# Optimization experiments

Measured on AMD Instinct MI355X. Metric: run time of the kernel, lower is better.

## Reference

```python
import jax, jax.numpy as jnp
import numpy as np

N_HID = 4
EPS = 1e-6  # LayerNorm eps (note: added to std, torch-style, std with ddof=1)


def _rnn_layer(wx_out, prev_pre, uh, g, b):
    """Sequential recurrence: at = wx_out[k] + h @ Uh^T; skip-subtract prev pre-act;
    custom layernorm (gamma*(x-mean)/(std+eps)+beta, std unbiased); relu.
    Returns (hiddens [T,B,H], pre_acts [T,B,H])."""
    T, B, H = wx_out.shape

    def step(h, inp):
        wx_k, prev_k = inp
        at = wx_k + h @ uh.T          # [B,H]
        pre = at
        a = at - prev_k               # skip connection (subtract prev layer pre-act)
        mean = a.mean(-1, keepdims=True)
        std = jnp.std(a, axis=-1, ddof=1, keepdims=True)
        a = g * (a - mean) / (std + EPS) + b
        h_new = jax.nn.relu(a)        # drop_mask = 1-drop_rate = 1.0 (test mode, drop_rate=0)
        return h_new, (h_new, pre)

    h0 = jnp.zeros((B, H), wx_out.dtype)
    _, (hs, pres) = jax.lax.scan(step, h0, (wx_out, prev_pre))
    return hs, pres


def setup_inputs() -> dict:
    key = jax.random.key(0)
    ks = jax.random.split(key, 12)
    T, B, D, H, C = 400, 32, 440, 1024, 3500
    s = 0.02
    return {
        "x": jax.random.normal(ks[0], (T, B, D), dtype=jnp.float32),
        "lab": jax.random.randint(ks[1], (T, B), 0, C),
        "test_flag": 1,
        "wx0_w": jax.random.normal(ks[2], (H, D), dtype=jnp.float32) * s,
        "wx0_b": jnp.zeros((H,), jnp.float32),
        "wx_w": jax.random.normal(ks[3], (N_HID - 1, H, H), dtype=jnp.float32) * s,
        "wx_b": jnp.zeros((N_HID - 1, H), jnp.float32),
        "uh_w": jax.random.normal(ks[4], (N_HID, H, H), dtype=jnp.float32) * s,
        "ln_g": jnp.ones((N_HID, H), jnp.float32),
        "ln_b": jnp.zeros((N_HID, H), jnp.float32),
        "fco_w": jax.random.normal(ks[5], (C, H), dtype=jnp.float32) * s,
        "fco_b": jnp.zeros((C,), jnp.float32),
    }


def reference(x, lab, test_flag, wx0_w, wx0_b, wx_w, wx_b, uh_w, ln_g, ln_b, fco_w, fco_b):
    T, B, _ = x.shape
    H = uh_w.shape[-1]
    prev_pre = jnp.zeros((T, B, H), x.dtype)  # skip_conn: layer 0 subtracts zeros
    h = x
    for i in range(N_HID):
        if i == 0:
            wx_out = jnp.einsum('tbd,hd->tbh', h, wx0_w) + wx0_b
        else:
            wx_out = jnp.einsum('tbd,hd->tbh', h, wx_w[i - 1]) + wx_b[i - 1]
        h, prev_pre = _rnn_layer(wx_out, prev_pre, uh_w[i], ln_g[i], ln_b[i])
    out = jnp.einsum('tbh,ch->tbc', h, fco_w) + fco_b   # [T,B,C]
    pout = jax.nn.log_softmax(out, axis=2)
    pred = jnp.argmax(pout, axis=2)
    nll = -jnp.take_along_axis(pout, lab[..., None], axis=2).squeeze(-1)
    loss = nll.mean()
    err = jnp.mean((pred != lab).astype(jnp.float32))
    return loss, err, pout
```

## Files before the change

kernel.cpp:

```cpp
#include <hip/hip_runtime.h>
#include <math.h>

#define T_STEPS 400
#define BATCH   32
#define HID     1024
#define MROWS   (T_STEPS * BATCH)
#define NCLS    3500
#define NG      8
#define BPG     4
#define CPG     32
#define JS      32
#define EPS     1e-6f
#define SLOTP   8

typedef __attribute__((ext_vector_type(8))) short short8v;
typedef __attribute__((ext_vector_type(4))) float f32x4;

__device__ __forceinline__ unsigned short bf16_rne(float x) {
  unsigned u = __builtin_bit_cast(unsigned, x);
  unsigned r = u + 0x7FFFu + ((u >> 16) & 1u);
  return (unsigned short)(r >> 16);
}

__device__ __forceinline__ void stage_tile(
    const float* __restrict__ src, int rowlim, int row0, int ld,
    int k0, int K, unsigned short* hi, unsigned short* lo, int tid) {
  #pragma unroll
  for (int it = 0; it < 2; ++it) {
    const int task = tid + 256 * it;
    const int r = task >> 2, q = task & 3;
    const int gr = row0 + r;
    const bool rok = gr < rowlim;
    const float* p = src + (size_t)gr * ld + k0 + q * 8;
    float x[8];
    if (rok && (k0 + 32 <= K)) {
      float4 v0 = *(const float4*)p;
      float4 v1 = *(const float4*)(p + 4);
      x[0] = v0.x; x[1] = v0.y; x[2] = v0.z; x[3] = v0.w;
      x[4] = v1.x; x[5] = v1.y; x[6] = v1.z; x[7] = v1.w;
    } else {
      #pragma unroll
      for (int j = 0; j < 8; ++j)
        x[j] = (rok && (k0 + q * 8 + j) < K) ? p[j] : 0.f;
    }
    unsigned hp[4], lp[4];
    #pragma unroll
    for (int j = 0; j < 4; ++j) {
      unsigned short h0 = bf16_rne(x[2 * j]), h1 = bf16_rne(x[2 * j + 1]);
      float f0 = __builtin_bit_cast(float, (unsigned)h0 << 16);
      float f1 = __builtin_bit_cast(float, (unsigned)h1 << 16);
      unsigned short l0 = bf16_rne(x[2 * j] - f0), l1 = bf16_rne(x[2 * j + 1] - f1);
      hp[j] = (unsigned)h0 | ((unsigned)h1 << 16);
      lp[j] = (unsigned)l0 | ((unsigned)l1 << 16);
    }
    const int idx = (r * 4 + (q ^ (r & 3))) * 8;
    *(uint4*)&hi[idx] = make_uint4(hp[0], hp[1], hp[2], hp[3]);
    *(uint4*)&lo[idx] = make_uint4(lp[0], lp[1], lp[2], lp[3]);
  }
}

template <int NPASS>
__global__ __launch_bounds__(256) void gemm_mfma(
    const float* __restrict__ A, const float* __restrict__ W,
    const float* __restrict__ bias, float* __restrict__ C,
    int M, int N, int K) {
  __shared__ unsigned short Ah[128 * 32], Al[128 * 32];
  __shared__ unsigned short Bh[128 * 32], Bl[128 * 32];
  const int tid = threadIdx.x;
  const int m0 = blockIdx.y * 128, n0 = blockIdx.x * 128;
  const int w = tid >> 6, lane = tid & 63;
  const int rlow = lane & 15, ksel = lane >> 4;

  f32x4 acc[8][2];
  #pragma unroll
  for (int i = 0; i < 8; ++i) {
    acc[i][0] = (f32x4)(0.f);
    acc[i][1] = (f32x4)(0.f);
  }

  for (int k0 = 0; k0 < K; k0 += 32) {
    __syncthreads();
    stage_tile(A, M, m0, K, k0, K, Ah, Al, tid);
    stage_tile(W, N, n0, K, k0, K, Bh, Bl, tid);
    __syncthreads();

    short8v wh[2], wl[2];
    #pragma unroll
    for (int nf = 0; nf < 2; ++nf) {
      const int rn = w * 32 + nf * 16 + rlow;
      const int idx = (rn * 4 + (ksel ^ (rn & 3))) * 8;
      wh[nf] = *(const short8v*)&Bh[idx];
      if (NPASS == 3) wl[nf] = *(const short8v*)&Bl[idx];
    }
    #pragma unroll
    for (int i = 0; i < 8; ++i) {
      const int ra = i * 16 + rlow;
      const int idx = (ra * 4 + (ksel ^ (ra & 3))) * 8;
      short8v ah = *(const short8v*)&Ah[idx];
      if (NPASS == 3) {
        short8v al = *(const short8v*)&Al[idx];
        acc[i][0] = __builtin_amdgcn_mfma_f32_16x16x32_bf16(ah, wh[0], acc[i][0], 0, 0, 0);
        acc[i][0] = __builtin_amdgcn_mfma_f32_16x16x32_bf16(al, wh[0], acc[i][0], 0, 0, 0);
        acc[i][0] = __builtin_amdgcn_mfma_f32_16x16x32_bf16(ah, wl[0], acc[i][0], 0, 0, 0);
        acc[i][1] = __builtin_amdgcn_mfma_f32_16x16x32_bf16(ah, wh[1], acc[i][1], 0, 0, 0);
        acc[i][1] = __builtin_amdgcn_mfma_f32_16x16x32_bf16(al, wh[1], acc[i][1], 0, 0, 0);
        acc[i][1] = __builtin_amdgcn_mfma_f32_16x16x32_bf16(ah, wl[1], acc[i][1], 0, 0, 0);
      } else {
        acc[i][0] = __builtin_amdgcn_mfma_f32_16x16x32_bf16(ah, wh[0], acc[i][0], 0, 0, 0);
        acc[i][1] = __builtin_amdgcn_mfma_f32_16x16x32_bf16(ah, wh[1], acc[i][1], 0, 0, 0);
      }
    }
  }

  int col[2]; float bb[2]; bool cok[2];
  #pragma unroll
  for (int nf = 0; nf < 2; ++nf) {
    col[nf] = n0 + w * 32 + nf * 16 + rlow;
    cok[nf] = col[nf] < N;
    bb[nf] = cok[nf] ? bias[col[nf]] : 0.f;
  }
  #pragma unroll
  for (int i = 0; i < 8; ++i) {
    const int row = m0 + i * 16 + ksel * 4;
    #pragma unroll
    for (int nf = 0; nf < 2; ++nf) {
      if (cok[nf]) {
        float* cp = C + (size_t)row * N + col[nf];
        cp[0 * N] = acc[i][nf][0] + bb[nf];
        cp[1 * N] = acc[i][nf][1] + bb[nf];
        cp[2 * N] = acc[i][nf][2] + bb[nf];
        cp[3 * N] = acc[i][nf][3] + bb[nf];
      }
    }
  }
}

__global__ void transpose1024(const float* __restrict__ in, float* __restrict__ out) {
  __shared__ float tile[32][33];
  const int bx = blockIdx.x * 32, by = blockIdx.y * 32;
  const int tx = threadIdx.x, ty = threadIdx.y;
  #pragma unroll
  for (int i = 0; i < 32; i += 8)
    tile[ty + i][tx] = in[(size_t)(by + ty + i) * HID + bx + tx];
  __syncthreads();
  #pragma unroll
  for (int i = 0; i < 32; i += 8)
    out[(size_t)(bx + ty + i) * HID + by + tx] = tile[tx][ty + i];
}

__global__ __launch_bounds__(256, 1) void scan_layer(
    const float* __restrict__ wx, const float* __restrict__ uhT,
    float* __restrict__ h_all, float* __restrict__ pre_all,
    float* __restrict__ a_pub,
    int* __restrict__ prog,
    const float* __restrict__ gamma, const float* __restrict__ beta,
    int skip_sub) {
  const int tid  = threadIdx.x;
  const int g    = blockIdx.x >> 5;
  const int c    = blockIdx.x & 31;
  const int lane = tid & 63;
  const int wv   = tid >> 6;
  const int jw   = tid & 3;
  const int ks   = tid >> 2;
  const int col0 = c * JS + jw * 8;

  int* prog_g = prog + (size_t)g * CPG * SLOTP;

  __shared__ float h_lds[HID * BPG];
  __shared__ float a_lds[BPG * HID];
  __shared__ float partial[4][BPG][JS];
  __shared__ float stats_lds[BPG][2];
  __shared__ float g_lds[HID], be_lds[HID];

  for (int k = tid; k < HID; k += 256) { g_lds[k] = gamma[k]; be_lds[k] = beta[k]; }

  float4 u0[16], u1[16];
  #pragma unroll
  for (int i = 0; i < 16; ++i) {
    const float* p = uhT + (size_t)(ks + 64 * i) * HID + col0;
    u0[i] = *(const float4*)p;
    u1[i] = *(const float4*)(p + 4);
  }
  __syncthreads();

  float at0 = 0.f, pre_old = 0.f;
  size_t gidx = 0;
  if (tid < 128) {
    const int b = tid >> 5, j = tid & 31;
    gidx = ((size_t)0 * BATCH + g * BPG + b) * HID + c * JS + j;
    at0 = wx[gidx];
    pre_old = skip_sub ? 0.f : pre_all[gidx];
  }

  for (int t = 0; t < T_STEPS; ++t) {
    const int par = t & 1;
    float* apub_t = a_pub + ((size_t)par * NG + g) * (BPG * HID);

    if (t > 0) {
      float pacc[4][8];
      #pragma unroll
      for (int b = 0; b < 4; ++b)
        #pragma unroll
        for (int q = 0; q < 8; ++q) pacc[b][q] = 0.f;
      #pragma unroll
      for (int i = 0; i < 16; ++i) {
        float4 h4 = *(const float4*)&h_lds[(ks + 64 * i) * 4];
        #pragma unroll
        for (int b = 0; b < 4; ++b) {
          float hb = ((const float*)&h4)[b];
          pacc[b][0] += hb * u0[i].x; pacc[b][1] += hb * u0[i].y;
          pacc[b][2] += hb * u0[i].z; pacc[b][3] += hb * u0[i].w;
          pacc[b][4] += hb * u1[i].x; pacc[b][5] += hb * u1[i].y;
          pacc[b][6] += hb * u1[i].z; pacc[b][7] += hb * u1[i].w;
        }
      }
      #pragma unroll
      for (int b = 0; b < 4; ++b)
        #pragma unroll
        for (int q = 0; q < 8; ++q) {
          float v = pacc[b][q];
          v += __shfl_xor(v, 4);
          v += __shfl_xor(v, 8);
          v += __shfl_xor(v, 16);
          v += __shfl_xor(v, 32);
          pacc[b][q] = v;
        }
      if ((lane >> 2) == 0) {
        #pragma unroll
        for (int b = 0; b < 4; ++b) {
          *(float4*)&partial[wv][b][jw * 8]     = *(const float4*)&pacc[b][0];
          *(float4*)&partial[wv][b][jw * 8 + 4] = *(const float4*)&pacc[b][4];
        }
      }
    }
    __syncthreads();

    if (tid < 128) {
      const int b = tid >> 5, j = tid & 31;
      float red = 0.f;
      if (t > 0)
        red = partial[0][b][j] + partial[1][b][j] + partial[2][b][j] + partial[3][b][j];
      float at = at0 + red;
      pre_all[gidx] = at;
      __hip_atomic_store(&apub_t[(size_t)b * HID + c * JS + j], at - pre_old,
                         __ATOMIC_RELAXED, __HIP_MEMORY_SCOPE_AGENT);
    }
    asm volatile("s_waitcnt vmcnt(0)" ::: "memory");
    __syncthreads();

    if (tid == 0)
      __hip_atomic_store(&prog_g[c * SLOTP], t + 1,
                         __ATOMIC_RELAXED, __HIP_MEMORY_SCOPE_AGENT);

    float at0_n = 0.f, pre_n = 0.f;
    size_t gidx_n = gidx;
    if (t + 1 < T_STEPS && tid < 128) {
      const int b = tid >> 5, j = tid & 31;
      gidx_n = ((size_t)(t + 1) * BATCH + g * BPG + b) * HID + c * JS + j;
      at0_n = wx[gidx_n];
      pre_n = skip_sub ? 0.f : pre_all[gidx_n];
    }

    {
      const int* p = &prog_g[(lane & 31) * SLOTP];
      while (true) {
        int v = __hip_atomic_load(p, __ATOMIC_RELAXED, __HIP_MEMORY_SCOPE_AGENT);
        if (__all(v >= t + 1)) break;
        __builtin_amdgcn_s_sleep(1);
      }
    }

    {
      float tmp[16];
      #pragma unroll
      for (int j = 0; j < 16; ++j)
        tmp[j] = __hip_atomic_load(&apub_t[tid + 256 * j],
                                   __ATOMIC_RELAXED, __HIP_MEMORY_SCOPE_AGENT);
      #pragma unroll
      for (int j = 0; j < 16; ++j)
        a_lds[tid + 256 * j] = tmp[j];
    }
    __syncthreads();

    {
      float s1 = 0.f, s2 = 0.f;
      #pragma unroll
      for (int i = 0; i < 16; ++i) {
        float v = a_lds[wv * HID + i * 64 + lane];
        s1 += v; s2 += v * v;
      }
      #pragma unroll
      for (int m = 1; m <= 32; m <<= 1) { s1 += __shfl_xor(s1, m); s2 += __shfl_xor(s2, m); }
      if (lane == 0) {
        float mean = s1 * (1.f / HID);
        float var = (s2 - (float)HID * mean * mean) * (1.f / (float)(HID - 1));
        stats_lds[wv][0] = mean;
        stats_lds[wv][1] = sqrtf(fmaxf(var, 0.f)) + EPS;
      }
    }
    __syncthreads();

    {
      float mean0 = stats_lds[0][0], rd0 = 1.f / stats_lds[0][1];
      float mean1 = stats_lds[1][0], rd1 = 1.f / stats_lds[1][1];
      float mean2 = stats_lds[2][0], rd2 = 1.f / stats_lds[2][1];
      float mean3 = stats_lds[3][0], rd3 = 1.f / stats_lds[3][1];
      #pragma unroll
      for (int j = 0; j < 4; ++j) {
        const int k = tid + 256 * j;
        float gk = g_lds[k], bk = be_lds[k];
        float h0 = fmaxf(gk * (a_lds[0 * HID + k] - mean0) * rd0 + bk, 0.f);
        float h1 = fmaxf(gk * (a_lds[1 * HID + k] - mean1) * rd1 + bk, 0.f);
        float h2 = fmaxf(gk * (a_lds[2 * HID + k] - mean2) * rd2 + bk, 0.f);
        float h3 = fmaxf(gk * (a_lds[3 * HID + k] - mean3) * rd3 + bk, 0.f);
        *(float4*)&h_lds[k * 4] = make_float4(h0, h1, h2, h3);
        if (c == 0) {
          h_all[((size_t)t * BATCH + g * BPG + 0) * HID + k] = h0;
          h_all[((size_t)t * BATCH + g * BPG + 1) * HID + k] = h1;
          h_all[((size_t)t * BATCH + g * BPG + 2) * HID + k] = h2;
          h_all[((size_t)t * BATCH + g * BPG + 3) * HID + k] = h3;
        }
      }
    }
    __syncthreads();

    at0 = at0_n; pre_old = pre_n; gidx = gidx_n;
  }
}

__global__ __launch_bounds__(256) void softmax_loss(
    float* __restrict__ out, const int* __restrict__ lab, float* __restrict__ acc) {
  __shared__ float rowbuf[NCLS];
  __shared__ float rv[4]; __shared__ int ri[4]; __shared__ float rs[4];
  __shared__ float shv[2];
  __shared__ int shidx;
  const int m = blockIdx.x;
  float* row = out + (size_t)m * NCLS;
  const int tid = threadIdx.x;
  const int lane = tid & 63, wid = tid >> 6;

  float vmax = -1e30f; int vidx = 0x7fffffff;
  for (int c2 = tid; c2 < NCLS / 2; c2 += 256) {
    float2 v = *(const float2*)(row + 2 * c2);
    rowbuf[2 * c2] = v.x; rowbuf[2 * c2 + 1] = v.y;
    if (v.x > vmax) { vmax = v.x; vidx = 2 * c2; }
    if (v.y > vmax) { vmax = v.y; vidx = (v.x > v.y) ? vidx : 2 * c2 + 1; }
  }
  #pragma unroll
  for (int off = 32; off; off >>= 1) {
    float ov = __shfl_down(vmax, off);
    int oi = __shfl_down(vidx, off);
    if (ov > vmax || (ov == vmax && oi < vidx)) { vmax = ov; vidx = oi; }
  }
  if (lane == 0) { rv[wid] = vmax; ri[wid] = vidx; }
  __syncthreads();
  if (tid == 0) {
    float bm = rv[0]; int bi = ri[0];
    for (int w = 1; w < 4; ++w)
      if (rv[w] > bm || (rv[w] == bm && ri[w] < bi)) { bm = rv[w]; bi = ri[w]; }
    shv[0] = bm; shidx = bi;
  }
  __syncthreads();
  float gmax = shv[0];
  float s = 0.f;
  for (int c = tid; c < NCLS; c += 256) s += expf(rowbuf[c] - gmax);
  #pragma unroll
  for (int off = 32; off; off >>= 1) s += __shfl_down(s, off);
  if (lane == 0) rs[wid] = s;
  __syncthreads();
  if (tid == 0) shv[1] = rs[0] + rs[1] + rs[2] + rs[3];
  __syncthreads();
  float lse = logf(shv[1]);
  for (int c2 = tid; c2 < NCLS / 2; c2 += 256) {
    float2 v;
    v.x = rowbuf[2 * c2] - gmax - lse;
    v.y = rowbuf[2 * c2 + 1] - gmax - lse;
    *(float2*)(row + 2 * c2) = v;
  }
  if (tid == 0) {
    int lb = lab[m];
    float nll = -(rowbuf[lb] - gmax - lse);
    atomicAdd(acc + 0, nll);
    atomicAdd(acc + 1, (shidx != lb) ? 1.f : 0.f);
  }
}

__global__ void init_acc(float* acc) { acc[threadIdx.x] = 0.f; }

__global__ void finalize_out(const float* __restrict__ acc, float* __restrict__ out) {
  out[0] = acc[0] * (1.f / (float)MROWS);
  out[1] = acc[1] * (1.f / (float)MROWS);
}

extern "C" void kernel_launch(void* const* d_in, const int* in_sizes, int n_in,
                              void* d_out, int out_size, void* d_ws, size_t ws_size,
                              hipStream_t stream) {
  const float* x     = (const float*)d_in[0];
  const int*   lab   = (const int*)d_in[1];
  const float* wx0_w = (const float*)d_in[3];
  const float* wx0_b = (const float*)d_in[4];
  const float* wx_w  = (const float*)d_in[5];
  const float* wx_b  = (const float*)d_in[6];
  const float* uh_w  = (const float*)d_in[7];
  const float* ln_g  = (const float*)d_in[8];
  const float* ln_b  = (const float*)d_in[9];
  const float* fco_w = (const float*)d_in[10];
  const float* fco_b = (const float*)d_in[11];
  float* out = (float*)d_out;

  float* wsf = (float*)d_ws;
  size_t off = 0;
  auto carve = [&](size_t n) { float* p = wsf + off; off += (n + 63) & ~(size_t)63; return p; };
  float* uhT   = carve((size_t)HID * HID);
  float* wxbuf = carve((size_t)MROWS * HID);
  float* h_all = carve((size_t)MROWS * HID);
  float* pre   = carve((size_t)MROWS * HID);
  float* a_pub = carve((size_t)2 * NG * BPG * HID);
  int*   prog  = (int*)carve((size_t)4 * NG * CPG * SLOTP);
  float* acc   = carve(64);

  (void)hipMemsetAsync(prog, 0, (size_t)4 * NG * CPG * SLOTP * sizeof(int), stream);
  init_acc<<<1, 2, 0, stream>>>(acc);

  for (int layer = 0; layer < 4; ++layer) {
    if (layer == 0) {
      gemm_mfma<3><<<dim3(HID / 128, MROWS / 128), 256, 0, stream>>>(
          x, wx0_w, wx0_b, wxbuf, MROWS, HID, 440);
    } else {
      gemm_mfma<3><<<dim3(HID / 128, MROWS / 128), 256, 0, stream>>>(
          h_all, wx_w + (size_t)(layer - 1) * HID * HID,
          wx_b + (size_t)(layer - 1) * HID, wxbuf, MROWS, HID, HID);
    }
    transpose1024<<<dim3(32, 32), dim3(32, 8), 0, stream>>>(
        uh_w + (size_t)layer * HID * HID, uhT);

    scan_layer<<<dim3(NG * CPG), 256, 0, stream>>>(
        wxbuf, uhT, h_all, pre, a_pub, prog + (size_t)layer * NG * CPG * SLOTP,
        ln_g + (size_t)layer * HID, ln_b + (size_t)layer * HID,
        (layer == 0) ? 1 : 0);
  }

  gemm_mfma<1><<<dim3((NCLS + 127) / 128, MROWS / 128), 256, 0, stream>>>(
      h_all, fco_w, fco_b, out + 2, MROWS, NCLS, HID);
  softmax_loss<<<MROWS, 256, 0, stream>>>(out + 2, lab, acc);
  finalize_out<<<1, 1, 0, stream>>>(acc, out);
}
```

Baseline: 10.32 ms.

## Fuse layer pairs into one wavefront-pipelined persistent scan kernel

Two consecutive RNN layers now run in a single persistent kernel, skewed by one timestep. Layer B's input projection (Wx) is computed on the fly from layer A's hidden state using register-resident weights, stored as packed bf16 hi/lo pairs. This halves the scan launches and grid-wide barriers, drops the middle input GEMM and the Uh transposes, and shares each step's barrier between both layers. In exchange, per-step compute and register pressure roughly triple, the weights are loaded with strided uncoalesced reads, and the split-bf16 form slightly reduces weight precision.

```diff
diff --git a/kernel.cpp b/kernel.cpp
--- a/kernel.cpp
+++ b/kernel.cpp
@@ -20,6 +20,18 @@
   unsigned u = __builtin_bit_cast(unsigned, x);
   unsigned r = u + 0x7FFFu + ((u >> 16) & 1u);
   return (unsigned short)(r >> 16);
+}
+
+__device__ __forceinline__ unsigned pack_w(float x) {
+  unsigned short h = bf16_rne(x);
+  float fh = __builtin_bit_cast(float, (unsigned)h << 16);
+  unsigned short l = bf16_rne(x - fh);
+  return ((unsigned)h << 16) | (unsigned)l;
+}
+__device__ __forceinline__ float unpk_w(unsigned u) {
+  float hi = __builtin_bit_cast(float, u & 0xFFFF0000u);
+  float lo = __builtin_bit_cast(float, u << 16);
+  return hi + lo;
 }
 
 __device__ __forceinline__ void stage_tile(
@@ -135,25 +147,19 @@
   }
 }
 
-__global__ void transpose1024(const float* __restrict__ in, float* __restrict__ out) {
-  __shared__ float tile[32][33];
-  const int bx = blockIdx.x * 32, by = blockIdx.y * 32;
-  const int tx = threadIdx.x, ty = threadIdx.y;
-  #pragma unroll
-  for (int i = 0; i < 32; i += 8)
-    tile[ty + i][tx] = in[(size_t)(by + ty + i) * HID + bx + tx];
-  __syncthreads();
-  #pragma unroll
-  for (int i = 0; i < 32; i += 8)
-    out[(size_t)(bx + ty + i) * HID + by + tx] = tile[tx][ty + i];
-}
-
-__global__ __launch_bounds__(256, 1) void scan_layer(
-    const float* __restrict__ wx, const float* __restrict__ uhT,
-    float* __restrict__ h_all, float* __restrict__ pre_all,
+__global__ __launch_bounds__(256, 1) void scan_pair(
+    const float* __restrict__ wx,
+    const float* __restrict__ ua_w,
+    const float* __restrict__ ub_w,
+    const float* __restrict__ wb_w,
+    const float* __restrict__ wb_bias,
+    float* __restrict__ h_all,
+    float* __restrict__ pre_prev,
+    float* __restrict__ pre_out,
     float* __restrict__ a_pub,
     int* __restrict__ prog,
-    const float* __restrict__ gamma, const float* __restrict__ beta,
+    const float* __restrict__ g_a, const float* __restrict__ be_a,
+    const float* __restrict__ g_b, const float* __restrict__ be_b,
     int skip_sub) {
   const int tid  = threadIdx.x;
   const int g    = blockIdx.x >> 5;
@@ -166,37 +172,60 @@
 
   int* prog_g = prog + (size_t)g * CPG * SLOTP;
 
-  __shared__ float h_lds[HID * BPG];
+  __shared__ float h_a_lds[HID * BPG];
+  __shared__ float h_b_lds[HID * BPG];
   __shared__ float a_lds[BPG * HID];
-  __shared__ float partial[4][BPG][JS];
+  __shared__ float partial_a[4][BPG][JS];
+  __shared__ float partial_b[4][BPG][JS];
   __shared__ float stats_lds[BPG][2];
-  __shared__ float g_lds[HID], be_lds[HID];
-
-  for (int k = tid; k < HID; k += 256) { g_lds[k] = gamma[k]; be_lds[k] = beta[k]; }
-
-  float4 u0[16], u1[16];
+
+  float4 ua0[16], ua1[16], ub0[16], ub1[16];
+  uint4  wp0[16], wp1[16];
   #pragma unroll
   for (int i = 0; i < 16; ++i) {
-    const float* p = uhT + (size_t)(ks + 64 * i) * HID + col0;
-    u0[i] = *(const float4*)p;
-    u1[i] = *(const float4*)(p + 4);
+    const int kk = ks + 64 * i;
+    float a0[8], b0[8], w0[8];
+    #pragma unroll
+    for (int q = 0; q < 8; ++q) {
+      const size_t off = (size_t)(col0 + q) * HID + kk;
+      a0[q] = ua_w[off];
+      b0[q] = ub_w[off];
+      w0[q] = wb_w[off];
+    }
+    ua0[i] = make_float4(a0[0], a0[1], a0[2], a0[3]);
+    ua1[i] = make_float4(a0[4], a0[5], a0[6], a0[7]);
+    ub0[i] = make_float4(b0[0], b0[1], b0[2], b0[3]);
+    ub1[i] = make_float4(b0[4], b0[5], b0[6], b0[7]);
+    wp0[i] = make_uint4(pack_w(w0[0]), pack_w(w0[1]), pack_w(w0[2]), pack_w(w0[3]));
+    wp1[i] = make_uint4(pack_w(w0[4]), pack_w(w0[5]), pack_w(w0[6]), pack_w(w0[7]));
+  }
+  float ga[4], ba[4], gb[4], bb[4];
+  #pragma unroll
+  for (int j = 0; j < 4; ++j) {
+    const int kk = tid + 256 * j;
+    ga[j] = g_a[kk]; ba[j] = be_a[kk];
+    gb[j] = g_b[kk]; bb[j] = be_b[kk];
+  }
+  float biasb = 0.f;
+  if (tid < 128) biasb = wb_bias[c * JS + (tid & 31)];
+
+  float wxa_r = 0.f, prev_r = 0.f, pre_a_reg = 0.f;
+  if (tid < 128) {
+    const size_t gi = ((size_t)0 * BATCH + g * BPG + (tid >> 5)) * HID + c * JS + (tid & 31);
+    wxa_r = wx[gi];
+    if (!skip_sub)
+      prev_r = __hip_atomic_load(&pre_prev[gi], __ATOMIC_RELAXED, __HIP_MEMORY_SCOPE_AGENT);
   }
   __syncthreads();
 
-  float at0 = 0.f, pre_old = 0.f;
-  size_t gidx = 0;
-  if (tid < 128) {
-    const int b = tid >> 5, j = tid & 31;
-    gidx = ((size_t)0 * BATCH + g * BPG + b) * HID + c * JS + j;
-    at0 = wx[gidx];
-    pre_old = skip_sub ? 0.f : pre_all[gidx];
-  }
-
-  for (int t = 0; t < T_STEPS; ++t) {
-    const int par = t & 1;
-    float* apub_t = a_pub + ((size_t)par * NG + g) * (BPG * HID);
-
-    if (t > 0) {
+  for (int k = 0; k <= T_STEPS; ++k) {
+    const int par = k & 1;
+    float* pa = a_pub + ((size_t)(par * 2 + 0) * NG + g) * (BPG * HID);
+    float* pb = a_pub + ((size_t)(par * 2 + 1) * NG + g) * (BPG * HID);
+    const bool doA = (k < T_STEPS);
+    const bool doB = (k >= 1);
+
+    if (doA && k > 0) {
       float pacc[4][8];
       #pragma unroll
       for (int b = 0; b < 4; ++b)
@@ -204,14 +233,14 @@
         for (int q = 0; q < 8; ++q) pacc[b][q] = 0.f;
       #pragma unroll
       for (int i = 0; i < 16; ++i) {
-        float4 h4 = *(const float4*)&h_lds[(ks + 64 * i) * 4];
+        float4 h4 = *(const float4*)&h_a_lds[(ks + 64 * i) * 4];
         #pragma unroll
         for (int b = 0; b < 4; ++b) {
           float hb = ((const float*)&h4)[b];
-          pacc[b][0] += hb * u0[i].x; pacc[b][1] += hb * u0[i].y;
-          pacc[b][2] += hb * u0[i].z; pacc[b][3] += hb * u0[i].w;
-          pacc[b][4] += hb * u1[i].x; pacc[b][5] += hb * u1[i].y;
-          pacc[b][6] += hb * u1[i].z; pacc[b][7] += hb * u1[i].w;
+          pacc[b][0] += hb * ua0[i].x; pacc[b][1] += hb * ua0[i].y;
+          pacc[b][2] += hb * ua0[i].z; pacc[b][3] += hb * ua0[i].w;
+          pacc[b][4] += hb * ua1[i].x; pacc[b][5] += hb * ua1[i].y;
+          pacc[b][6] += hb * ua1[i].z; pacc[b][7] += hb * ua1[i].w;
         }
       }
       #pragma unroll
@@ -219,17 +248,65 @@
         #pragma unroll
         for (int q = 0; q < 8; ++q) {
           float v = pacc[b][q];
-          v += __shfl_xor(v, 4);
-          v += __shfl_xor(v, 8);
-          v += __shfl_xor(v, 16);
-          v += __shfl_xor(v, 32);
+          v += __shfl_xor(v, 4); v += __shfl_xor(v, 8);
+          v += __shfl_xor(v, 16); v += __shfl_xor(v, 32);
           pacc[b][q] = v;
         }
       if ((lane >> 2) == 0) {
         #pragma unroll
         for (int b = 0; b < 4; ++b) {
-          *(float4*)&partial[wv][b][jw * 8]     = *(const float4*)&pacc[b][0];
-          *(float4*)&partial[wv][b][jw * 8 + 4] = *(const float4*)&pacc[b][4];
+          *(float4*)&partial_a[wv][b][jw * 8]     = *(const float4*)&pacc[b][0];
+          *(float4*)&partial_a[wv][b][jw * 8 + 4] = *(const float4*)&pacc[b][4];
+        }
+      }
+    }
+
+    if (doB) {
+      float pacc[4][8];
+      #pragma unroll
+      for (int b = 0; b < 4; ++b)
+        #pragma unroll
+        for (int q = 0; q < 8; ++q) pacc[b][q] = 0.f;
+      #pragma unroll
+      for (int i = 0; i < 16; ++i) {
+        float4 ha = *(const float4*)&h_a_lds[(ks + 64 * i) * 4];
+        float w[8];
+        w[0] = unpk_w(wp0[i].x); w[1] = unpk_w(wp0[i].y);
+        w[2] = unpk_w(wp0[i].z); w[3] = unpk_w(wp0[i].w);
+        w[4] = unpk_w(wp1[i].x); w[5] = unpk_w(wp1[i].y);
+        w[6] = unpk_w(wp1[i].z); w[7] = unpk_w(wp1[i].w);
+        #pragma unroll
+        for (int b = 0; b < 4; ++b) {
+          float hv = ((const float*)&ha)[b];
+          #pragma unroll
+          for (int q = 0; q < 8; ++q) pacc[b][q] += hv * w[q];
+        }
+        if (k >= 2) {
+          float4 hb4 = *(const float4*)&h_b_lds[(ks + 64 * i) * 4];
+          #pragma unroll
+          for (int b = 0; b < 4; ++b) {
+            float hv = ((const float*)&hb4)[b];
+            pacc[b][0] += hv * ub0[i].x; pacc[b][1] += hv * ub0[i].y;
+            pacc[b][2] += hv * ub0[i].z; pacc[b][3] += hv * ub0[i].w;
+            pacc[b][4] += hv * ub1[i].x; pacc[b][5] += hv * ub1[i].y;
+            pacc[b][6] += hv * ub1[i].z; pacc[b][7] += hv * ub1[i].w;
+          }
+        }
+      }
+      #pragma unroll
+      for (int b = 0; b < 4; ++b)
+        #pragma unroll
+        for (int q = 0; q < 8; ++q) {
+          float v = pacc[b][q];
+          v += __shfl_xor(v, 4); v += __shfl_xor(v, 8);
+          v += __shfl_xor(v, 16); v += __shfl_xor(v, 32);
+          pacc[b][q] = v;
+        }
+      if ((lane >> 2) == 0) {
+        #pragma unroll
+        for (int b = 0; b < 4; ++b) {
+          *(float4*)&partial_b[wv][b][jw * 8]     = *(const float4*)&pacc[b][0];
+          *(float4*)&partial_b[wv][b][jw * 8 + 4] = *(const float4*)&pacc[b][4];
         }
       }
     }
@@ -237,94 +314,153 @@
 
     if (tid < 128) {
       const int b = tid >> 5, j = tid & 31;
-      float red = 0.f;
-      if (t > 0)
-        red = partial[0][b][j] + partial[1][b][j] + partial[2][b][j] + partial[3][b][j];
-      float at = at0 + red;
-      pre_all[gidx] = at;
-      __hip_atomic_store(&apub_t[(size_t)b * HID + c * JS + j], at - pre_old,
-                         __ATOMIC_RELAXED, __HIP_MEMORY_SCOPE_AGENT);
+      float at_a_new = 0.f;
+      if (doA) {
+        float red = 0.f;
+        if (k > 0)
+          red = partial_a[0][b][j] + partial_a[1][b][j]
+              + partial_a[2][b][j] + partial_a[3][b][j];
+        at_a_new = wxa_r + red;
+        __hip_atomic_store(&pa[(size_t)b * HID + c * JS + j], at_a_new - prev_r,
+                           __ATOMIC_RELAXED, __HIP_MEMORY_SCOPE_AGENT);
+      }
+      if (doB) {
+        float redb = partial_b[0][b][j] + partial_b[1][b][j]
+                   + partial_b[2][b][j] + partial_b[3][b][j];
+        float at_b = biasb + redb;
+        const size_t gib = ((size_t)(k - 1) * BATCH + g * BPG + b) * HID + c * JS + j;
+        __hip_atomic_store(&pre_out[gib], at_b,
+                           __ATOMIC_RELAXED, __HIP_MEMORY_SCOPE_AGENT);
+        __hip_atomic_store(&pb[(size_t)b * HID + c * JS + j], at_b - pre_a_reg,
+                           __ATOMIC_RELAXED, __HIP_MEMORY_SCOPE_AGENT);
+      }
+      if (doA) pre_a_reg = at_a_new;
     }
     asm volatile("s_waitcnt vmcnt(0)" ::: "memory");
     __syncthreads();
 
     if (tid == 0)
-      __hip_atomic_store(&prog_g[c * SLOTP], t + 1,
+      __hip_atomic_store(&prog_g[c * SLOTP], k + 1,
                          __ATOMIC_RELAXED, __HIP_MEMORY_SCOPE_AGENT);
 
-    float at0_n = 0.f, pre_n = 0.f;
-    size_t gidx_n = gidx;
-    if (t + 1 < T_STEPS && tid < 128) {
-      const int b = tid >> 5, j = tid & 31;
-      gidx_n = ((size_t)(t + 1) * BATCH + g * BPG + b) * HID + c * JS + j;
-      at0_n = wx[gidx_n];
-      pre_n = skip_sub ? 0.f : pre_all[gidx_n];
+    float wxa_n = 0.f, prev_n = 0.f;
+    if (k + 1 < T_STEPS && tid < 128) {
+      const size_t gi = ((size_t)(k + 1) * BATCH + g * BPG + (tid >> 5)) * HID
+                        + c * JS + (tid & 31);
+      wxa_n = wx[gi];
+      if (!skip_sub)
+        prev_n = __hip_atomic_load(&pre_prev[gi], __ATOMIC_RELAXED, __HIP_MEMORY_SCOPE_AGENT);
     }
 
     {
       const int* p = &prog_g[(lane & 31) * SLOTP];
       while (true) {
         int v = __hip_atomic_load(p, __ATOMIC_RELAXED, __HIP_MEMORY_SCOPE_AGENT);
-        if (__all(v >= t + 1)) break;
+        if (__all(v >= k + 1)) break;
         __builtin_amdgcn_s_sleep(1);
       }
     }
 
-    {
-      float tmp[16];
+    float ta[16], tb[16];
+    if (doA) {
       #pragma unroll
       for (int j = 0; j < 16; ++j)
-        tmp[j] = __hip_atomic_load(&apub_t[tid + 256 * j],
-                                   __ATOMIC_RELAXED, __HIP_MEMORY_SCOPE_AGENT);
+        ta[j] = __hip_atomic_load(&pa[tid + 256 * j],
+                                  __ATOMIC_RELAXED, __HIP_MEMORY_SCOPE_AGENT);
+    }
+    if (doB) {
       #pragma unroll
       for (int j = 0; j < 16; ++j)
-        a_lds[tid + 256 * j] = tmp[j];
+        tb[j] = __hip_atomic_load(&pb[tid + 256 * j],
+                                  __ATOMIC_RELAXED, __HIP_MEMORY_SCOPE_AGENT);
+    }
+
+    if (doA) {
+      #pragma unroll
+      for (int j = 0; j < 16; ++j) a_lds[tid + 256 * j] = ta[j];
+      __syncthreads();
+      {
+        float s1 = 0.f, s2 = 0.f;
+        #pragma unroll
+        for (int i = 0; i < 16; ++i) {
+          float v = a_lds[wv * HID + i * 64 + lane];
+          s1 += v; s2 += v * v;
+        }
+        #pragma unroll
+        for (int m = 1; m <= 32; m <<= 1) { s1 += __shfl_xor(s1, m); s2 += __shfl_xor(s2, m); }
+        if (lane == 0) {
+          float mean = s1 * (1.f / HID);
+          float var = (s2 - (float)HID * mean * mean) * (1.f / (float)(HID - 1));
+          stats_lds[wv][0] = mean;
+          stats_lds[wv][1] = sqrtf(fmaxf(var, 0.f)) + EPS;
+        }
+      }
+      __syncthreads();
+      {
+        float m0 = stats_lds[0][0], r0 = 1.f / stats_lds[0][1];
+        float m1 = stats_lds[1][0], r1 = 1.f / stats_lds[1][1];
+        float m2 = stats_lds[2][0], r2 = 1.f / stats_lds[2][1];
+        float m3 = stats_lds[3][0], r3 = 1.f / stats_lds[3][1];
+        #pragma unroll
+        for (int j = 0; j < 4; ++j) {
+          const int kk = tid + 256 * j;
+          float h0 = fmaxf(ga[j] * (a_lds[0 * HID + kk] - m0) * r0 + ba[j], 0.f);
+          float h1 = fmaxf(ga[j] * (a_lds[1 * HID + kk] - m1) * r1 + ba[j], 0.f);
+          float h2 = fmaxf(ga[j] * (a_lds[2 * HID + kk] - m2) * r2 + ba[j], 0.f);
+          float h3 = fmaxf(ga[j] * (a_lds[3 * HID + kk] - m3) * r3 + ba[j], 0.f);
+          *(float4*)&h_a_lds[kk * 4] = make_float4(h0, h1, h2, h3);
+        }
+      }
+      __syncthreads();
+    }
+
+    if (doB) {
+      #pragma unroll
+      for (int j = 0; j < 16; ++j) a_lds[tid + 256 * j] = tb[j];
+      __syncthreads();
+      {
+        float s1 = 0.f, s2 = 0.f;
+        #pragma unroll
+        for (int i = 0; i < 16; ++i) {
+          float v = a_lds[wv * HID + i * 64 + lane];
+          s1 += v; s2 += v * v;
+        }
+        #pragma unroll
+        for (int m = 1; m <= 32; m <<= 1) { s1 += __shfl_xor(s1, m); s2 += __shfl_xor(s2, m); }
+        if (lane == 0) {
+          float mean = s1 * (1.f / HID);
+          float var = (s2 - (float)HID * mean * mean) * (1.f / (float)(HID - 1));
+          stats_lds[wv][0] = mean;
+          stats_lds[wv][1] = sqrtf(fmaxf(var, 0.f)) + EPS;
+        }
+      }
+      __syncthreads();
+      {
+        float m0 = stats_lds[0][0], r0 = 1.f / stats_lds[0][1];
+        float m1 = stats_lds[1][0], r1 = 1.f / stats_lds[1][1];
+        float m2 = stats_lds[2][0], r2 = 1.f / stats_lds[2][1];
+        float m3 = stats_lds[3][0], r3 = 1.f / stats_lds[3][1];
+        #pragma unroll
+        for (int j = 0; j < 4; ++j) {
+          const int kk = tid + 256 * j;
+          float h0 = fmaxf(gb[j] * (a_lds[0 * HID + kk] - m0) * r0 + bb[j], 0.f);
+          float h1 = fmaxf(gb[j] * (a_lds[1 * HID + kk] - m1) * r1 + bb[j], 0.f);
+          float h2 = fmaxf(gb[j] * (a_lds[2 * HID + kk] - m2) * r2 + bb[j], 0.f);
+          float h3 = fmaxf(gb[j] * (a_lds[3 * HID + kk] - m3) * r3 + bb[j], 0.f);
+          *(float4*)&h_b_lds[kk * 4] = make_float4(h0, h1, h2, h3);
+          if (c == 0) {
+            const size_t hb0 = ((size_t)(k - 1) * BATCH + g * BPG) * HID + kk;
+            h_all[hb0 + 0 * HID] = h0;
+            h_all[hb0 + 1 * HID] = h1;
+            h_all[hb0 + 2 * HID] = h2;
+            h_all[hb0 + 3 * HID] = h3;
+          }
+        }
+      }
     }
     __syncthreads();
 
-    {
-      float s1 = 0.f, s2 = 0.f;
-      #pragma unroll
-      for (int i = 0; i < 16; ++i) {
-        float v = a_lds[wv * HID + i * 64 + lane];
-        s1 += v; s2 += v * v;
-      }
-      #pragma unroll
-      for (int m = 1; m <= 32; m <<= 1) { s1 += __shfl_xor(s1, m); s2 += __shfl_xor(s2, m); }
-      if (lane == 0) {
-        float mean = s1 * (1.f / HID);
-        float var = (s2 - (float)HID * mean * mean) * (1.f / (float)(HID - 1));
-        stats_lds[wv][0] = mean;
-        stats_lds[wv][1] = sqrtf(fmaxf(var, 0.f)) + EPS;
-      }
-    }
-    __syncthreads();
-
-    {
-      float mean0 = stats_lds[0][0], rd0 = 1.f / stats_lds[0][1];
-      float mean1 = stats_lds[1][0], rd1 = 1.f / stats_lds[1][1];
-      float mean2 = stats_lds[2][0], rd2 = 1.f / stats_lds[2][1];
-      float mean3 = stats_lds[3][0], rd3 = 1.f / stats_lds[3][1];
-      #pragma unroll
-      for (int j = 0; j < 4; ++j) {
-        const int k = tid + 256 * j;
-        float gk = g_lds[k], bk = be_lds[k];
-        float h0 = fmaxf(gk * (a_lds[0 * HID + k] - mean0) * rd0 + bk, 0.f);
-        float h1 = fmaxf(gk * (a_lds[1 * HID + k] - mean1) * rd1 + bk, 0.f);
-        float h2 = fmaxf(gk * (a_lds[2 * HID + k] - mean2) * rd2 + bk, 0.f);
-        float h3 = fmaxf(gk * (a_lds[3 * HID + k] - mean3) * rd3 + bk, 0.f);
-        *(float4*)&h_lds[k * 4] = make_float4(h0, h1, h2, h3);
-        if (c == 0) {
-          h_all[((size_t)t * BATCH + g * BPG + 0) * HID + k] = h0;
-          h_all[((size_t)t * BATCH + g * BPG + 1) * HID + k] = h1;
-          h_all[((size_t)t * BATCH + g * BPG + 2) * HID + k] = h2;
-          h_all[((size_t)t * BATCH + g * BPG + 3) * HID + k] = h3;
-        }
-      }
-    }
-    __syncthreads();
-
-    at0 = at0_n; pre_old = pre_n; gidx = gidx_n;
+    wxa_r = wxa_n; prev_r = prev_n;
   }
 }
 
@@ -411,34 +547,31 @@
   float* wsf = (float*)d_ws;
   size_t off = 0;
   auto carve = [&](size_t n) { float* p = wsf + off; off += (n + 63) & ~(size_t)63; return p; };
-  float* uhT   = carve((size_t)HID * HID);
   float* wxbuf = carve((size_t)MROWS * HID);
   float* h_all = carve((size_t)MROWS * HID);
   float* pre   = carve((size_t)MROWS * HID);
-  float* a_pub = carve((size_t)2 * NG * BPG * HID);
-  int*   prog  = (int*)carve((size_t)4 * NG * CPG * SLOTP);
+  float* a_pub = carve((size_t)2 * 2 * NG * BPG * HID);
+  int*   prog  = (int*)carve((size_t)2 * NG * CPG * SLOTP);
   float* acc   = carve(64);
 
-  (void)hipMemsetAsync(prog, 0, (size_t)4 * NG * CPG * SLOTP * sizeof(int), stream);
+  (void)hipMemsetAsync(prog, 0, (size_t)2 * NG * CPG * SLOTP * sizeof(int), stream);
   init_acc<<<1, 2, 0, stream>>>(acc);
 
-  for (int layer = 0; layer < 4; ++layer) {
-    if (layer == 0) {
-      gemm_mfma<3><<<dim3(HID / 128, MROWS / 128), 256, 0, stream>>>(
-          x, wx0_w, wx0_b, wxbuf, MROWS, HID, 440);
-    } else {
-      gemm_mfma<3><<<dim3(HID / 128, MROWS / 128), 256, 0, stream>>>(
-          h_all, wx_w + (size_t)(layer - 1) * HID * HID,
-          wx_b + (size_t)(layer - 1) * HID, wxbuf, MROWS, HID, HID);
-    }
-    transpose1024<<<dim3(32, 32), dim3(32, 8), 0, stream>>>(
-        uh_w + (size_t)layer * HID * HID, uhT);
-
-    scan_layer<<<dim3(NG * CPG), 256, 0, stream>>>(
-        wxbuf, uhT, h_all, pre, a_pub, prog + (size_t)layer * NG * CPG * SLOTP,
-        ln_g + (size_t)layer * HID, ln_b + (size_t)layer * HID,
-        (layer == 0) ? 1 : 0);
-  }
+  const size_t HH = (size_t)HID * HID;
+
+  gemm_mfma<3><<<dim3(HID / 128, MROWS / 128), 256, 0, stream>>>(
+      x, wx0_w, wx0_b, wxbuf, MROWS, HID, 440);
+  scan_pair<<<dim3(NG * CPG), 256, 0, stream>>>(
+      wxbuf, uh_w + 0 * HH, uh_w + 1 * HH, wx_w + 0 * HH, wx_b + 0 * HID,
+      h_all, pre , pre, a_pub, prog,
+      ln_g + 0 * HID, ln_b + 0 * HID, ln_g + 1 * HID, ln_b + 1 * HID, 1);
+
+  gemm_mfma<3><<<dim3(HID / 128, MROWS / 128), 256, 0, stream>>>(
+      h_all, wx_w + 1 * HH, wx_b + 1 * HID, wxbuf, MROWS, HID, HID);
+  scan_pair<<<dim3(NG * CPG), 256, 0, stream>>>(
+      wxbuf, uh_w + 2 * HH, uh_w + 3 * HH, wx_w + 2 * HH, wx_b + 2 * HID,
+      h_all, pre , pre, a_pub, prog + (size_t)NG * CPG * SLOTP,
+      ln_g + 2 * HID, ln_b + 2 * HID, ln_g + 3 * HID, ln_b + 3 * HID, 0);
 
   gemm_mfma<1><<<dim3((NCLS + 127) / 128, MROWS / 128), 256, 0, stream>>>(
       h_all, fco_w, fco_b, out + 2, MROWS, NCLS, HID);
```

After: 11.08 ms. 1.07x slower.
